# Optimization experiments

Measured on AMD Instinct MI355X. Metric: run time of the kernel, lower is better.

Reference implementation:

```python
import jax, jax.numpy as jnp
import numpy as np

B, S, IN_DIM, P_DIM, H = 2, 2048, 1024, 512, 8
HD = P_DIM // H
N_PENTA = 1024
SCALES = (128, 256, 512)
K_NEIGH = max(16, min(int(S * 0.15), 128))  # adaptive window -> 128
SCALE = 1.0 / float(np.sqrt(HD))
EPS = 1e-5


def _ln(x, g, b):
    mu = jnp.mean(x, axis=-1, keepdims=True)
    var = jnp.mean((x - mu) ** 2, axis=-1, keepdims=True)
    return (x - mu) * jax.lax.rsqrt(var + EPS) * g + b


def setup_inputs() -> dict:
    key = jax.random.key(0)
    ks = list(jax.random.split(key, 6 + 2 * len(SCALES)))
    w = lambda k, shp: jax.random.normal(k, shp, jnp.float32) * 0.02
    inp = {
        'sequence_features': jax.random.normal(ks[0], (B, S, IN_DIM), jnp.float32),
        'shared_pentachora': jax.random.normal(ks[1], (N_PENTA, 5, P_DIM), jnp.float32),
        'shared_positions': jax.random.uniform(ks[2], (N_PENTA,), dtype=jnp.float32),
        'proj_W': w(ks[3], (IN_DIM, P_DIM)), 'proj_b': jnp.zeros((P_DIM,), jnp.float32),
        'ln_g': jnp.ones((P_DIM,), jnp.float32), 'ln_b': jnp.zeros((P_DIM,), jnp.float32),
        'qkv_W': w(ks[4], (P_DIM, 3 * P_DIM)), 'qkv_b': jnp.zeros((3 * P_DIM,), jnp.float32),
        'out_W': w(ks[5], (P_DIM, P_DIM)), 'out_b': jnp.zeros((P_DIM,), jnp.float32),
    }
    i = 6
    for s in SCALES:
        inp[f'w1_{s}'] = w(ks[i], (P_DIM, 2 * s)); inp[f'b1_{s}'] = jnp.zeros((2 * s,), jnp.float32)
        inp[f'g_{s}'] = jnp.ones((2 * s,), jnp.float32); inp[f'bb_{s}'] = jnp.zeros((2 * s,), jnp.float32)
        inp[f'w2_{s}'] = w(ks[i + 1], (2 * s, s)); inp[f'b2_{s}'] = jnp.zeros((s,), jnp.float32)
        i += 2
    return inp


def _attend_one(z_b, pos_b, qkv_W, qkv_b, out_W, out_b):
    # z_b: [S, P_DIM], pos_b: [S]
    qkv = (z_b @ qkv_W + qkv_b).reshape(S, 3, H, HD)
    q = jnp.transpose(qkv[:, 0], (1, 0, 2))  # [H, S, HD]
    k = jnp.transpose(qkv[:, 1], (1, 0, 2))
    v = jnp.transpose(qkv[:, 2], (1, 0, 2))
    dist = jnp.abs(pos_b[:, None] - pos_b[None, :])  # [S, S]
    _, routes = jax.lax.top_k(-dist, K_NEIGH)        # [S, K] nearest in Cantor space
    kg = k[:, routes, :]  # [H, S, K, HD] gathered keys
    vg = v[:, routes, :]
    scores = jnp.einsum('hqd,hqkd->hqk', q, kg) * SCALE
    attn = jax.nn.softmax(scores, axis=-1)
    out = jnp.einsum('hqk,hqkd->hqd', attn, vg)
    out = jnp.transpose(out, (1, 0, 2)).reshape(S, P_DIM)
    return out @ out_W + out_b


def reference(sequence_features, shared_pentachora, shared_positions, proj_W, proj_b, ln_g, ln_b, qkv_W, qkv_b, out_W, out_b, w1_128, b1_128, g_128, bb_128, w2_128, b2_128, w1_256, b1_256, g_256, bb_256, w2_256, b2_256, w1_512, b1_512, g_512, bb_512, w2_512, b2_512):
    # centroids from pentachora vertices, L2-normalized
    cent = shared_pentachora.mean(axis=1)
    cent = cent / jnp.clip(jnp.linalg.norm(cent, axis=-1, keepdims=True), 1e-12)
    # input projection -> LN -> GELU -> L2 normalize
    z = jax.nn.gelu(_ln(sequence_features @ proj_W + proj_b, ln_g, ln_b), approximate=False)
    z = z / jnp.clip(jnp.linalg.norm(z, axis=-1, keepdims=True), 1e-12)
    # match to opinion anchors, inherit Cantor positions
    anchor_ids = jnp.argmax(jnp.einsum('bnd,pd->bnp', z, cent), axis=-1)  # [B, S]
    cantor_positions = shared_positions[anchor_ids]  # [B, S]
    # per-sample geometric sparse attention (vmapped over batch)
    z_att = jax.vmap(_attend_one, in_axes=(0, 0, None, None, None, None))(
        z, cantor_positions, qkv_W, qkv_b, out_W, out_b)  # [B, S, P_DIM]
    pooled = z_att.mean(axis=1)  # [B, P_DIM] (no attention mask)
    scale_params = (
        (w1_128, b1_128, g_128, bb_128, w2_128, b2_128),
        (w1_256, b1_256, g_256, bb_256, w2_256, b2_256),
        (w1_512, b1_512, g_512, bb_512, w2_512, b2_512),
    )
    outs = []
    for (w1, b1, g, bb, w2, b2) in scale_params:
        h = jax.nn.gelu(_ln(pooled @ w1 + b1, g, bb), approximate=False)
        outs.append(h @ w2 + b2)
    return jnp.concatenate(outs, axis=-1)  # [B, 128+256+512] concatenated scale opinions
```

## Files before the change

kernel.cpp:

```cpp
#include <hip/hip_runtime.h>
#include <math.h>

#define DEV __device__ __forceinline__

static constexpr int S_LEN  = 2048;
static constexpr int IN_DIM = 1024;
static constexpr int P_DIM  = 512;
static constexpr int NHEAD  = 8;
static constexpr int HD     = 64;
static constexpr int KN     = 128;

typedef __attribute__((ext_vector_type(8))) short bf16x8;
typedef __attribute__((ext_vector_type(4))) float f32x4;

DEV float gelu_exact(float x) {
    return 0.5f * x * (1.0f + erff(x * 0.70710678118654752440f));
}

DEV short bf_hi(float x) {
    unsigned u = __float_as_uint(x);
    unsigned r = (u + 0x7fffu + ((u >> 16) & 1u)) >> 16;
    return (short)r;
}
DEV float bf_f(short h) { return __uint_as_float(((unsigned)(unsigned short)h) << 16); }

DEV float block_reduce_sum(float v, float* sm4) {
    #pragma unroll
    for (int off = 32; off; off >>= 1) v += __shfl_down(v, off, 64);
    int lane = threadIdx.x & 63, w = threadIdx.x >> 6;
    __syncthreads();
    if (lane == 0) sm4[w] = v;
    __syncthreads();
    return sm4[0] + sm4[1] + sm4[2] + sm4[3];
}

__global__ __launch_bounds__(256) void k_cent(const float* __restrict__ penta,
                                              short* __restrict__ ch,
                                              short* __restrict__ cl) {
    int p = blockIdx.x, t = threadIdx.x;
    __shared__ float sm4[4];
    float c0 = 0.f, c1 = 0.f;
    #pragma unroll
    for (int v = 0; v < 5; v++) {
        const float* row = penta + ((long)p * 5 + v) * P_DIM;
        c0 += row[t];
        c1 += row[t + 256];
    }
    c0 /= 5.0f; c1 /= 5.0f;
    float tot = block_reduce_sum(c0 * c0 + c1 * c1, sm4);
    float n = fmaxf(sqrtf(tot), 1e-12f);
    float v0 = c0 / n, v1 = c1 / n;
    short h0 = bf_hi(v0), h1 = bf_hi(v1);
    ch[p * P_DIM + t]       = h0;
    ch[p * P_DIM + t + 256] = h1;
    cl[p * P_DIM + t]       = bf_hi(v0 - bf_f(h0));
    cl[p * P_DIM + t + 256] = bf_hi(v1 - bf_f(h1));
}

template <int K, int N>
__global__ __launch_bounds__(256) void k_wt(const float* __restrict__ W,
                                            short* __restrict__ WTh,
                                            short* __restrict__ WTl) {
    __shared__ float tile[64][65];
    int bk = blockIdx.x, bn = blockIdx.y;
    int t = threadIdx.x;
    int c = t & 63, r4 = t >> 6;
    #pragma unroll
    for (int i = 0; i < 16; i++) {
        int row = r4 + i * 4;
        tile[row][c] = W[(long)(bk * 64 + row) * N + bn * 64 + c];
    }
    __syncthreads();
    #pragma unroll
    for (int i = 0; i < 16; i++) {
        int n = r4 + i * 4;
        float v = tile[c][n];
        short h = bf_hi(v);
        long o = (long)(bn * 64 + n) * K + bk * 64 + c;
        WTh[o] = h;
        WTl[o] = bf_hi(v - bf_f(h));
    }
}

template <int BM, int K, int N, int EPI, bool SPLITA>
__global__ __launch_bounds__(256) void k_mm(const float* __restrict__ Af,
                                            const short* __restrict__ Ash,
                                            const short* __restrict__ Asl,
                                            const short* __restrict__ BTh,
                                            const short* __restrict__ BTl,
                                            const float* __restrict__ bias,
                                            float* __restrict__ C,
                                            unsigned long long* __restrict__ rowkey) {
    constexpr int TI = (BM + 31) / 32;
    __shared__ short Ah[BM * 40], Al[BM * 40], Bh[128 * 40], Bl[128 * 40];
    int t = threadIdx.x;
    int lane = t & 63, wave = t >> 6;
    int wr = (wave >> 1) * (BM / 2), wc = (wave & 1) * 64;
    int m = lane & 15, quad = lane >> 4;
    int rb = blockIdx.x * BM, cb = blockIdx.y * 128;

    f32x4 acc[TI][4];
    #pragma unroll
    for (int i = 0; i < TI; i++)
        #pragma unroll
        for (int j = 0; j < 4; j++) acc[i][j] = (f32x4){0.f, 0.f, 0.f, 0.f};

    for (int k0 = 0; k0 < K; k0 += 32) {
        __syncthreads();
        if constexpr (SPLITA) {
            constexpr int TOT = BM * 4;
            #pragma unroll
            for (int ps = 0; ps < (TOT + 255) / 256; ps++) {
                int idx = t + ps * 256;
                if (idx < TOT) {
                    int row = idx >> 2, c4 = idx & 3;
                    *(float4*)(Ah + row * 40 + c4 * 8) =
                        *(const float4*)(Ash + (long)(rb + row) * K + k0 + c4 * 8);
                    *(float4*)(Al + row * 40 + c4 * 8) =
                        *(const float4*)(Asl + (long)(rb + row) * K + k0 + c4 * 8);
                }
            }
        } else {
            #pragma unroll
            for (int ps = 0; ps < BM / 32; ps++) {
                int row = (t >> 3) + ps * 32;
                int seg = t & 7;
                float4 v = *(const float4*)(Af + (long)(rb + row) * K + k0 + seg * 4);
                short h0 = bf_hi(v.x), h1 = bf_hi(v.y), h2 = bf_hi(v.z), h3 = bf_hi(v.w);
                short l0 = bf_hi(v.x - bf_f(h0)), l1 = bf_hi(v.y - bf_f(h1));
                short l2 = bf_hi(v.z - bf_f(h2)), l3 = bf_hi(v.w - bf_f(h3));
                *(short4*)(Ah + row * 40 + seg * 4) = make_short4(h0, h1, h2, h3);
                *(short4*)(Al + row * 40 + seg * 4) = make_short4(l0, l1, l2, l3);
            }
        }
        #pragma unroll
        for (int ps = 0; ps < 2; ps++) {
            int row = (t >> 2) + ps * 64;
            int seg = t & 3;
            *(float4*)(Bh + row * 40 + seg * 8) =
                *(const float4*)(BTh + (long)(cb + row) * K + k0 + seg * 8);
            *(float4*)(Bl + row * 40 + seg * 8) =
                *(const float4*)(BTl + (long)(cb + row) * K + k0 + seg * 8);
        }
        __syncthreads();

        bf16x8 ah[TI], al[TI], bh[4], bl[4];
        #pragma unroll
        for (int i = 0; i < TI; i++) {
            ah[i] = *(const bf16x8*)(Ah + (wr + i * 16 + m) * 40 + quad * 8);
            al[i] = *(const bf16x8*)(Al + (wr + i * 16 + m) * 40 + quad * 8);
        }
        #pragma unroll
        for (int j = 0; j < 4; j++) {
            bh[j] = *(const bf16x8*)(Bh + (wc + j * 16 + m) * 40 + quad * 8);
            bl[j] = *(const bf16x8*)(Bl + (wc + j * 16 + m) * 40 + quad * 8);
        }
        #pragma unroll
        for (int i = 0; i < TI; i++)
            #pragma unroll
            for (int j = 0; j < 4; j++) {
                acc[i][j] = __builtin_amdgcn_mfma_f32_16x16x32_bf16(ah[i], bh[j], acc[i][j], 0, 0, 0);
                acc[i][j] = __builtin_amdgcn_mfma_f32_16x16x32_bf16(ah[i], bl[j], acc[i][j], 0, 0, 0);
                acc[i][j] = __builtin_amdgcn_mfma_f32_16x16x32_bf16(al[i], bh[j], acc[i][j], 0, 0, 0);
            }
    }

    if (EPI == 0) {
        #pragma unroll
        for (int i = 0; i < TI; i++) {
            int gr0 = rb + wr + i * 16 + quad * 4;
            #pragma unroll
            for (int j = 0; j < 4; j++) {
                int gc = cb + wc + j * 16 + m;
                float bv = bias[gc];
                #pragma unroll
                for (int r = 0; r < 4; r++)
                    C[(long)(gr0 + r) * N + gc] = acc[i][j][r] + bv;
            }
        }
    } else {
        #pragma unroll
        for (int i = 0; i < TI; i++) {
            #pragma unroll
            for (int r = 0; r < 4; r++) {
                int gr = rb + wr + i * 16 + quad * 4 + r;
                float bv = acc[i][0][r];
                int bp = cb + wc + m;
                #pragma unroll
                for (int j = 1; j < 4; j++) {
                    float v = acc[i][j][r];
                    int p = cb + wc + j * 16 + m;
                    if (v > bv) { bv = v; bp = p; }
                }
                #pragma unroll
                for (int off = 1; off < 16; off <<= 1) {
                    float ov = __shfl_xor(bv, off, 64);
                    int op = __shfl_xor(bp, off, 64);
                    if (ov > bv || (ov == bv && op < bp)) { bv = ov; bp = op; }
                }
                if (m == 0) {
                    unsigned u = __float_as_uint(bv);
                    u = (u & 0x80000000u) ? ~u : (u | 0x80000000u);
                    unsigned long long key =
                        ((unsigned long long)u << 32) | (unsigned)(0xFFFFFFFFu - (unsigned)bp);
                    atomicMax(&rowkey[gr], key);
                }
            }
        }
    }
}

__global__ __launch_bounds__(256) void k_ln_gelu_norm(const float* __restrict__ Zin,
                                                      const float* __restrict__ g,
                                                      const float* __restrict__ b,
                                                      short* __restrict__ z_h,
                                                      short* __restrict__ z_l) {
    long row = blockIdx.x;
    int t = threadIdx.x;
    __shared__ float sm4[4];
    float x0 = Zin[row * P_DIM + t], x1 = Zin[row * P_DIM + t + 256];
    float mu = block_reduce_sum(x0 + x1, sm4) * (1.0f / P_DIM);
    float d0 = x0 - mu, d1 = x1 - mu;
    float var = block_reduce_sum(d0 * d0 + d1 * d1, sm4) * (1.0f / P_DIM);
    float rs = 1.0f / sqrtf(var + 1e-5f);
    float y0 = gelu_exact(d0 * rs * g[t] + b[t]);
    float y1 = gelu_exact(d1 * rs * g[t + 256] + b[t + 256]);
    float nn = block_reduce_sum(y0 * y0 + y1 * y1, sm4);
    float n = fmaxf(sqrtf(nn), 1e-12f);
    float v0 = y0 / n, v1 = y1 / n;
    short h0 = bf_hi(v0), h1 = bf_hi(v1);
    z_h[row * P_DIM + t]       = h0;
    z_h[row * P_DIM + t + 256] = h1;
    z_l[row * P_DIM + t]       = bf_hi(v0 - bf_f(h0));
    z_l[row * P_DIM + t + 256] = bf_hi(v1 - bf_f(h1));
}

__global__ __launch_bounds__(1024) void k_sort(const unsigned long long* __restrict__ rowkey,
                                               const float* __restrict__ spos,
                                               int* __restrict__ order,
                                               float* __restrict__ pos_srt) {
    int b = blockIdx.x, t = threadIdx.x;
    __shared__ unsigned long long key[2048];
    for (int u = 0; u < 2; u++) {
        int i = t + u * 1024;
        unsigned p = 0xFFFFFFFFu - (unsigned)(rowkey[b * 2048 + i] & 0xFFFFFFFFull);
        float pv = spos[p];
        key[i] = (((unsigned long long)__float_as_uint(pv)) << 32) | (unsigned)i;
    }
    __syncthreads();
    for (int k = 2; k <= 2048; k <<= 1) {
        for (int j = k >> 1; j > 0; j >>= 1) {
            for (int u = 0; u < 2; u++) {
                int i = t + u * 1024;
                int l = i ^ j;
                if (l > i) {
                    bool up = ((i & k) == 0);
                    unsigned long long a = key[i], c = key[l];
                    if ((a > c) == up) { key[i] = c; key[l] = a; }
                }
            }
            __syncthreads();
        }
    }
    for (int u = 0; u < 2; u++) {
        int r = t + u * 1024;
        unsigned long long kk = key[r];
        order[b * 2048 + r]   = (int)(kk & 0xffffffffu);
        pos_srt[b * 2048 + r] = __uint_as_float((unsigned)(kk >> 32));
    }
}

__global__ __launch_bounds__(256) void k_routes(const float* __restrict__ pos_srt,
                                                const int* __restrict__ order,
                                                unsigned long long* __restrict__ bmG,
                                                uint2* __restrict__ bounds) {
    int blk = blockIdx.x;
    int b = blk >> 9;
    int t = threadIdx.x;
    int lane = t & 63, wave = t >> 6;
    int r = (blk & 511) * 4 + wave;
    __shared__ float ps[2048];
    __shared__ unsigned short tk[2048];
    for (int u = 0; u < 8; u++) {
        int i = t + u * 256;
        ps[i] = pos_srt[b * 2048 + i];
        tk[i] = (unsigned short)order[b * 2048 + i];
    }
    __syncthreads();

    float pi = ps[r];
    float T = 3e38f;
    #pragma unroll
    for (int a2 = 0; a2 < 2; a2++) {
        int a = lane + a2 * 64;
        int jl = r - a, jr = r + 127 - a;
        if (jl >= 0 && jr <= 2047) {
            float dl = (a > 0)   ? (pi - ps[jl]) : 0.f;
            float dr = (a < 127) ? (ps[jr] - pi) : 0.f;
            T = fminf(T, fmaxf(dl, dr));
        }
    }
    #pragma unroll
    for (int off = 1; off < 64; off <<= 1) T = fminf(T, __shfl_xor(T, off, 64));

    int lo = 0, hi = r;
    while (lo < hi) { int mid = (lo + hi) >> 1; if (pi - ps[mid] <= T) hi = mid; else lo = mid + 1; }
    int mn = lo;
    lo = r; hi = 2047;
    while (lo < hi) { int mid = (lo + hi + 1) >> 1; if (ps[mid] - pi <= T) lo = mid; else hi = mid - 1; }
    int mx = lo;
    int Ls, Rs;
    if (T > 0.f) {
        lo = 0; hi = r;
        while (lo < hi) { int mid = (lo + hi) >> 1; if (pi - ps[mid] < T) hi = mid; else lo = mid + 1; }
        Ls = lo;
        lo = r; hi = 2047;
        while (lo < hi) { int mid = (lo + hi + 1) >> 1; if (ps[mid] - pi < T) lo = mid; else hi = mid - 1; }
        Rs = lo;
    } else { Ls = r + 1; Rs = r - 1; }

    int cnt_strict = (Rs >= Ls) ? (Rs - Ls + 1) : 0;
    int need = 128 - cnt_strict;
    int l0a, l0b, r0a, r0b;
    if (cnt_strict > 0) { l0a = mn; l0b = Ls - 1; r0a = Rs + 1; r0b = mx; }
    else                { l0a = mn; l0b = mx;     r0a = 1;      r0b = 0; }
    int nL = (l0b >= l0a) ? (l0b - l0a + 1) : 0;
    int nR = (r0b >= r0a) ? (r0b - r0a + 1) : 0;
    int tiecount = nL + nR;

    int X = 65535;
    if (need < tiecount) {
        int lo2 = 0, hi2 = 2047;
        while (lo2 < hi2) {
            int mid = (lo2 + hi2) >> 1;
            int cnt = 0;
            for (int e = lane; e < tiecount; e += 64) {
                int j = (e < nL) ? (l0a + e) : (r0a + e - nL);
                cnt += (tk[j] <= mid) ? 1 : 0;
            }
            #pragma unroll
            for (int off = 1; off < 64; off <<= 1) cnt += __shfl_xor(cnt, off, 64);
            if (cnt >= need) hi2 = mid; else lo2 = mid + 1;
        }
        X = lo2;
    }

    int qlo_loc = 1 << 30, qhi_loc = -1;
    if (lane < 32) {
        unsigned long long bits = 0;
        int j0 = lane << 6, j1 = j0 + 63;
        if (cnt_strict > 0) {
            int a0 = max(Ls, j0), a1 = min(Rs, j1);
            if (a0 <= a1) {
                int s = a0 - j0, e = a1 - j0;
                unsigned long long msk = (e - s == 63) ? ~0ull
                                       : (((1ull << (e - s + 1)) - 1) << s);
                bits |= msk;
            }
        }
        int a0 = max(l0a, j0), a1 = min(l0b, j1);
        for (int j = a0; j <= a1; j++) if (tk[j] <= X) bits |= 1ull << (j - j0);
        a0 = max(r0a, j0); a1 = min(r0b, j1);
        for (int j = a0; j <= a1; j++) if (tk[j] <= X) bits |= 1ull << (j - j0);
        if (bits) {
            qlo_loc = j0 + __builtin_ctzll(bits);
            qhi_loc = j0 + 63 - __builtin_clzll(bits);
        }
        bmG[((long)(b * 2048 + r)) * 32 + lane] = bits;
    }
    #pragma unroll
    for (int off = 1; off < 64; off <<= 1) {
        qlo_loc = min(qlo_loc, __shfl_xor(qlo_loc, off, 64));
        qhi_loc = max(qhi_loc, __shfl_xor(qhi_loc, off, 64));
    }
    if (lane == 0)
        bounds[b * 2048 + r] = make_uint2((unsigned)qlo_loc, (unsigned)qhi_loc);
}

__global__ __launch_bounds__(256) void k_kprep(const float* __restrict__ qkv,
                                               const int* __restrict__ order,
                                               short* __restrict__ Ks_h,
                                               short* __restrict__ Ks_l) {
    int b = blockIdx.y;
    int t = threadIdx.x;
    int lr = t >> 5;
    int seg = t & 31;
    int rank = blockIdx.x * 8 + lr;
    int tok = order[b * 2048 + rank];
    const float4* src = (const float4*)qkv + (long)(b * 2048 + tok) * 384 + 128 + seg * 4;
    long dsto = (long)(b * 2048 + rank) * 512 + seg * 16;
    #pragma unroll
    for (int u = 0; u < 4; u++) {
        float4 v = src[u];
        short h0 = bf_hi(v.x), h1 = bf_hi(v.y), h2 = bf_hi(v.z), h3 = bf_hi(v.w);
        *(short4*)(Ks_h + dsto + u * 4) = make_short4(h0, h1, h2, h3);
        *(short4*)(Ks_l + dsto + u * 4) =
            make_short4(bf_hi(v.x - bf_f(h0)), bf_hi(v.y - bf_f(h1)),
                        bf_hi(v.z - bf_f(h2)), bf_hi(v.w - bf_f(h3)));
    }
}

__global__ __launch_bounds__(256) void k_vprep(const float* __restrict__ qkv,
                                               const int* __restrict__ order,
                                               short* __restrict__ Vt_h) {
    __shared__ short tile[64][72];
    int rt = blockIdx.x, dt = blockIdx.y, b = blockIdx.z;
    int t = threadIdx.x;
    int lr = t >> 2;
    int q4 = t & 3;
    int tok = order[b * 2048 + rt * 64 + lr];
    const float4* src = (const float4*)qkv + (long)(b * 2048 + tok) * 384 + 256 + dt * 16;
    #pragma unroll
    for (int u = 0; u < 4; u++) {
        float4 v = src[q4 + u * 4];
        int d0 = (q4 + u * 4) * 4;
        tile[d0 + 0][lr] = bf_hi(v.x);
        tile[d0 + 1][lr] = bf_hi(v.y);
        tile[d0 + 2][lr] = bf_hi(v.z);
        tile[d0 + 3][lr] = bf_hi(v.w);
    }
    __syncthreads();
    int d = t >> 2, c4 = t & 3;
    long o = ((long)(b * 512 + dt * 64 + d)) * 2048 + rt * 64 + c4 * 16;
    #pragma unroll
    for (int j = 0; j < 4; j++)
        *(short4*)(Vt_h + o + j * 4) = make_short4(tile[d][c4 * 16 + j * 4 + 0],
                                                   tile[d][c4 * 16 + j * 4 + 1],
                                                   tile[d][c4 * 16 + j * 4 + 2],
                                                   tile[d][c4 * 16 + j * 4 + 3]);
}

__global__ __launch_bounds__(256) void k_attn(const float* __restrict__ qkv,
                                              const int* __restrict__ order,
                                              const unsigned long long* __restrict__ bmG,
                                              const uint2* __restrict__ bounds,
                                              const short* __restrict__ Ks_h,
                                              const short* __restrict__ Ks_l,
                                              const short* __restrict__ Vt_h,
                                              float* __restrict__ pooledZ) {
    __shared__ __align__(16) char smem[17280];
    short* Pt = (short*)smem;
    unsigned short* cm = (unsigned short*)(smem + 10240);
    float* Opart = (float*)smem;
    float2* ml = (float2*)(smem + 16384);
    int* sh_tok = (int*)(smem + 16896);
    int* sh_lohi = (int*)(smem + 16960);
    float2* sc = (float2*)(smem + 16968);

    int gb = blockIdx.x;
    int b  = gb >> 9;
    int qg = (gb >> 2) & 127;
    int hp = gb & 3;
    int h0 = hp * 2;
    int r0 = qg * 16;
    int t = threadIdx.x;
    int lane = t & 63, wave = t >> 6;
    int rh = wave & 1, hs = wave >> 1;
    int key = lane & 15, quad = lane >> 4;

    const float4* qkvF4 = (const float4*)qkv;

    if (t < 16) sh_tok[t] = order[b * 2048 + r0 + t];
    if (t == 0) { sh_lohi[0] = 1 << 30; sh_lohi[1] = 0; }
    #pragma unroll
    for (int u = 0; u < 8; u++) {
        int e = t + u * 256;
        int c = e >> 4, q = e & 15;
        cm[c * 16 + q] = (unsigned short)(
            (bmG[((long)(b * 2048 + r0 + q)) * 32 + (c >> 2)] >> ((c & 3) * 16)) & 0xFFFF);
    }
    __syncthreads();
    if (t < 16) {
        uint2 bd = bounds[b * 2048 + r0 + t];
        atomicMin(&sh_lohi[0], (int)bd.x);
        atomicMax(&sh_lohi[1], (int)bd.y);
    }

    bf16x8 qh[2], ql[2];
    {
        long tq = (long)(b * 2048 + sh_tok[key]) * 384;
        #pragma unroll
        for (int ks = 0; ks < 2; ks++) {
            float4 v0 = qkvF4[tq + (h0 + hs) * 16 + ks * 8 + quad * 2];
            float4 v1 = qkvF4[tq + (h0 + hs) * 16 + ks * 8 + quad * 2 + 1];
            float vv[8] = {v0.x, v0.y, v0.z, v0.w, v1.x, v1.y, v1.z, v1.w};
            #pragma unroll
            for (int j = 0; j < 8; j++) {
                short hb = bf_hi(vv[j]);
                qh[ks][j] = hb;
                ql[ks][j] = bf_hi(vv[j] - bf_f(hb));
            }
        }
    }
    __syncthreads();
    int lo = sh_lohi[0] & ~63, hi = sh_lohi[1] + 1;

    float mrow[4], lrow[4];
    f32x4 Ont[4];
    #pragma unroll
    for (int r = 0; r < 4; r++) { mrow[r] = -1e30f; lrow[r] = 0.f; }
    #pragma unroll
    for (int nt = 0; nt < 4; nt++) Ont[nt] = (f32x4){0.f, 0.f, 0.f, 0.f};

    short* PtH = Pt + wave * 1280;
    short* PtL = PtH + 640;

    int hd = h0 + hs;
    long kbase = ((long)b * 2048) * 512 + hd * 64 + quad * 8;
    long vbase = ((long)(b * 512 + hd * 64 + key)) * 2048;

    for (int c0 = lo; c0 < hi; c0 += 64) {
        int cb = c0 + rh * 32;
        if (cb >= hi) continue;
        int ch0 = cb >> 4;
        unsigned long long m0 = *(const unsigned long long*)(cm + ch0 * 16 + quad * 4);
        unsigned long long m1 = (ch0 + 1 < 128)
            ? *(const unsigned long long*)(cm + (ch0 + 1) * 16 + quad * 4) : 0ull;
        if (!__any((m0 | m1) != 0ull)) continue;

        long kr0 = kbase + (long)(cb + key) * 512;
        long kr1 = kbase + (long)(cb + 16 + key) * 512;

        f32x4 S0 = (f32x4){0.f,0.f,0.f,0.f}, S1 = (f32x4){0.f,0.f,0.f,0.f};
        #pragma unroll
        for (int ks = 0; ks < 2; ks++) {
            bf16x8 b0h = *(const bf16x8*)(Ks_h + kr0 + ks * 32);
            bf16x8 b0l = *(const bf16x8*)(Ks_l + kr0 + ks * 32);
            bf16x8 b1h = *(const bf16x8*)(Ks_h + kr1 + ks * 32);
            bf16x8 b1l = *(const bf16x8*)(Ks_l + kr1 + ks * 32);
            S0 = __builtin_amdgcn_mfma_f32_16x16x32_bf16(qh[ks], b0h, S0, 0, 0, 0);
            S0 = __builtin_amdgcn_mfma_f32_16x16x32_bf16(qh[ks], b0l, S0, 0, 0, 0);
            S0 = __builtin_amdgcn_mfma_f32_16x16x32_bf16(ql[ks], b0h, S0, 0, 0, 0);
            S1 = __builtin_amdgcn_mfma_f32_16x16x32_bf16(qh[ks], b1h, S1, 0, 0, 0);
            S1 = __builtin_amdgcn_mfma_f32_16x16x32_bf16(qh[ks], b1l, S1, 0, 0, 0);
            S1 = __builtin_amdgcn_mfma_f32_16x16x32_bf16(ql[ks], b1h, S1, 0, 0, 0);
        }
        float s0[4], s1[4], p0[4], p1[4];
        unsigned bit0[4], bit1[4];
        #pragma unroll
        for (int r = 0; r < 4; r++) {
            bit0[r] = (unsigned)((m0 >> (r * 16 + key)) & 1);
            bit1[r] = (unsigned)((m1 >> (r * 16 + key)) & 1);
            s0[r] = bit0[r] ? S0[r] * 0.125f : -1e30f;
            s1[r] = bit1[r] ? S1[r] * 0.125f : -1e30f;
        }
        #pragma unroll
        for (int r = 0; r < 4; r++) {
            float cmax = fmaxf(s0[r], s1[r]);
            cmax = fmaxf(cmax, __shfl_xor(cmax, 1, 64));
            cmax = fmaxf(cmax, __shfl_xor(cmax, 2, 64));
            cmax = fmaxf(cmax, __shfl_xor(cmax, 4, 64));
            cmax = fmaxf(cmax, __shfl_xor(cmax, 8, 64));
            float mn = fmaxf(mrow[r], cmax);
            float alpha = __expf(mrow[r] - mn);
            mrow[r] = mn;
            p0[r] = bit0[r] ? __expf(s0[r] - mn) : 0.f;
            p1[r] = bit1[r] ? __expf(s1[r] - mn) : 0.f;
            float rs = p0[r] + p1[r];
            rs += __shfl_xor(rs, 1, 64);
            rs += __shfl_xor(rs, 2, 64);
            rs += __shfl_xor(rs, 4, 64);
            rs += __shfl_xor(rs, 8, 64);
            lrow[r] = lrow[r] * alpha + rs;
            #pragma unroll
            for (int nt = 0; nt < 4; nt++) Ont[nt][r] *= alpha;
        }
        #pragma unroll
        for (int r = 0; r < 4; r++) {
            short ha = bf_hi(p0[r]);
            PtH[(quad * 4 + r) * 40 + key] = ha;
            PtL[(quad * 4 + r) * 40 + key] = bf_hi(p0[r] - bf_f(ha));
            short hb = bf_hi(p1[r]);
            PtH[(quad * 4 + r) * 40 + 16 + key] = hb;
            PtL[(quad * 4 + r) * 40 + 16 + key] = bf_hi(p1[r] - bf_f(hb));
        }
        bf16x8 pfh = *(const bf16x8*)(PtH + key * 40 + quad * 8);
        bf16x8 pfl = *(const bf16x8*)(PtL + key * 40 + quad * 8);
        #pragma unroll
        for (int nt = 0; nt < 4; nt++) {
            bf16x8 vf = *(const bf16x8*)(Vt_h + vbase + (long)nt * 16 * 2048
                                         + cb + quad * 8);
            Ont[nt] = __builtin_amdgcn_mfma_f32_16x16x32_bf16(pfh, vf, Ont[nt], 0, 0, 0);
            Ont[nt] = __builtin_amdgcn_mfma_f32_16x16x32_bf16(pfl, vf, Ont[nt], 0, 0, 0);
        }
    }

    if (key == 0) {
        #pragma unroll
        for (int r = 0; r < 4; r++)
            ml[(rh * 2 + hs) * 16 + quad * 4 + r] = make_float2(mrow[r], lrow[r]);
    }
    __syncthreads();
    #pragma unroll
    for (int nt = 0; nt < 4; nt++)
        #pragma unroll
        for (int r = 0; r < 4; r++)
            Opart[rh * 2048 + (quad * 4 + r) * 128 + hs * 64 + nt * 16 + key] = Ont[nt][r];

    if (t < 32) {
        int q = t >> 1, hs2 = t & 1;
        float2 a = ml[(0 * 2 + hs2) * 16 + q];
        float2 c = ml[(1 * 2 + hs2) * 16 + q];
        float M = fmaxf(a.x, c.x);
        float w0 = __expf(a.x - M), w1 = __expf(c.x - M);
        float inv = 1.0f / fmaxf(a.y * w0 + c.y * w1, 1e-37f);
        sc[hs2 * 16 + q] = make_float2(w0 * inv, w1 * inv);
    }
    __syncthreads();

    if (t < 128) {
        int d = t, hs2 = d >> 6;
        float s = 0.f;
        #pragma unroll
        for (int q = 0; q < 16; q++) {
            float2 w = sc[hs2 * 16 + q];
            s += Opart[q * 128 + d] * w.x + Opart[2048 + q * 128 + d] * w.y;
        }
        atomicAdd(&pooledZ[b * P_DIM + h0 * HD + d], s);
    }
}

__global__ __launch_bounds__(256) void k_opool(const float* __restrict__ pooledZ,
                                               const float* __restrict__ outW,
                                               const float* __restrict__ outb,
                                               float* __restrict__ pooled) {
    int b = blockIdx.y, t = threadIdx.x;
    int c = blockIdx.x * 256 + t;
    __shared__ float pz[P_DIM];
    pz[t]       = pooledZ[b * P_DIM + t];
    pz[t + 256] = pooledZ[b * P_DIM + t + 256];
    __syncthreads();
    float acc = 0.f;
    #pragma unroll 8
    for (int d = 0; d < P_DIM; d++) acc = fmaf(pz[d], outW[d * P_DIM + c], acc);
    pooled[b * P_DIM + c] = acc + (float)S_LEN * outb[c];
}

__global__ __launch_bounds__(256) void k_exp_fc1(const float* __restrict__ pooled,
                                                 const float* __restrict__ w1_0, const float* __restrict__ b1_0,
                                                 const float* __restrict__ w1_1, const float* __restrict__ b1_1,
                                                 const float* __restrict__ w1_2, const float* __restrict__ b1_2,
                                                 float* __restrict__ h) {
    int t = threadIdx.x, b = blockIdx.y;
    int c = blockIdx.x * 256 + t;
    __shared__ float pl[P_DIM];
    pl[t]       = pooled[b * P_DIM + t]       * (1.0f / S_LEN);
    pl[t + 256] = pooled[b * P_DIM + t + 256] * (1.0f / S_LEN);
    __syncthreads();

    const float* wp; const float* bp; int s2, j;
    if (c < 256)      { wp = w1_0; bp = b1_0; s2 = 256;  j = c; }
    else if (c < 768) { wp = w1_1; bp = b1_1; s2 = 512;  j = c - 256; }
    else              { wp = w1_2; bp = b1_2; s2 = 1024; j = c - 768; }

    const float* p = wp + j;
    float acc = 0.f;
    #pragma unroll 16
    for (int k = 0; k < P_DIM; k++) {
        acc = fmaf(pl[k], *p, acc);
        p += s2;
    }
    h[(long)b * 1792 + c] = acc + bp[j];
}

__global__ __launch_bounds__(256) void k_exp_ln(float* __restrict__ h,
                                                const float* __restrict__ g0, const float* __restrict__ bb0,
                                                const float* __restrict__ g1, const float* __restrict__ bb1,
                                                const float* __restrict__ g2, const float* __restrict__ bb2) {
    int e = blockIdx.x, b = blockIdx.y, t = threadIdx.x;
    __shared__ float sm4[4];
    const int offs[3] = {0, 256, 768};
    const int ns[3]   = {256, 512, 1024};
    const float* gs[3]  = {g0, g1, g2};
    const float* bbs[3] = {bb0, bb1, bb2};
    int n = ns[e];
    float* hp = h + (long)b * 1792 + offs[e];
    const float* g = gs[e]; const float* bb = bbs[e];

    float x[4];
    float loc = 0.f;
    for (int u = 0; u < 4; u++) {
        int j = t + u * 256;
        x[u] = (j < n) ? hp[j] : 0.f;
        loc += x[u];
    }
    float mu = block_reduce_sum(loc, sm4) / (float)n;
    loc = 0.f;
    for (int u = 0; u < 4; u++) {
        int j = t + u * 256;
        if (j < n) { float d = x[u] - mu; loc += d * d; }
    }
    float var = block_reduce_sum(loc, sm4) / (float)n;
    float rs = 1.0f / sqrtf(var + 1e-5f);
    for (int u = 0; u < 4; u++) {
        int j = t + u * 256;
        if (j < n) hp[j] = gelu_exact((x[u] - mu) * rs * g[j] + bb[j]);
    }
}

__global__ __launch_bounds__(256) void k_exp_fc2(const float* __restrict__ h,
                                                 const float* __restrict__ w2_0, const float* __restrict__ b2_0,
                                                 const float* __restrict__ w2_1, const float* __restrict__ b2_1,
                                                 const float* __restrict__ w2_2, const float* __restrict__ b2_2,
                                                 float* __restrict__ out) {
    int t = threadIdx.x, b = blockIdx.y;
    int c = blockIdx.x * 256 + t;
    __shared__ float hs[1792];
    for (int u = 0; u < 7; u++) hs[t + u * 256] = h[(long)b * 1792 + t + u * 256];
    __syncthreads();
    if (c >= 896) return;

    const float* wp; const float* bp; int s2, sN, j, off_h;
    if (c < 128)      { wp = w2_0; bp = b2_0; s2 = 256;  sN = 128; j = c;       off_h = 0; }
    else if (c < 384) { wp = w2_1; bp = b2_1; s2 = 512;  sN = 256; j = c - 128; off_h = 256; }
    else              { wp = w2_2; bp = b2_2; s2 = 1024; sN = 512; j = c - 384; off_h = 768; }

    const float* p = wp + j;
    const float* hh = hs + off_h;
    float acc = 0.f;
    #pragma unroll 16
    for (int k = 0; k < s2; k++) {
        acc = fmaf(hh[k], *p, acc);
        p += sN;
    }
    out[b * 896 + c] = acc + bp[j];
}

extern "C" void kernel_launch(void* const* d_in, const int* in_sizes, int n_in,
                              void* d_out, int out_size, void* d_ws, size_t ws_size,
                              hipStream_t stream) {
    const float* seq   = (const float*)d_in[0];
    const float* penta = (const float*)d_in[1];
    const float* spos  = (const float*)d_in[2];
    const float* projW = (const float*)d_in[3];
    const float* projb = (const float*)d_in[4];
    const float* lng   = (const float*)d_in[5];
    const float* lnb   = (const float*)d_in[6];
    const float* qkvW  = (const float*)d_in[7];
    const float* qkvb  = (const float*)d_in[8];
    const float* outW  = (const float*)d_in[9];
    const float* outb  = (const float*)d_in[10];

    float* ws      = (float*)d_ws;
    float* z_pre   = ws;
    short* z_h     = (short*)(z_pre + 2097152);
    short* z_l     = z_h + 2097152;
    float* qkv     = (float*)(z_l + 2097152);
    float* pooledZ = qkv + 6291456;
    float* pooled  = pooledZ + 4096;
    float* hbuf    = pooled + 1024;
    unsigned long long* rowkey = (unsigned long long*)(hbuf + 4096);
    float* pos_srt = (float*)(rowkey + 4096);
    int*   order   = (int*)(pos_srt + 4096);
    uint2* bounds  = (uint2*)(order + 4096);
    unsigned long long* bmG = (unsigned long long*)(bounds + 4096);
    short* cent_h  = (short*)(bmG + 131072);
    short* cent_l  = cent_h + 524288;
    short* pjWT_h  = cent_l + 524288;
    short* pjWT_l  = pjWT_h + 524288;
    short* qkWT_h  = pjWT_l + 524288;
    short* qkWT_l  = qkWT_h + 786432;

    short* Ks_h = (short*)z_pre;
    short* Ks_l = Ks_h + 2097152;
    short* Vt_h = cent_h;

    k_cent<<<1024, 256, 0, stream>>>(penta, cent_h, cent_l);
    { dim3 g(16, 8);  k_wt<IN_DIM, P_DIM><<<g, 256, 0, stream>>>(projW, pjWT_h, pjWT_l); }
    { dim3 g(8, 24);  k_wt<P_DIM, 3 * P_DIM><<<g, 256, 0, stream>>>(qkvW, qkWT_h, qkWT_l); }

    { dim3 g(128, 4); k_mm<32, IN_DIM, P_DIM, 0, false><<<g, 256, 0, stream>>>(
          seq, nullptr, nullptr, pjWT_h, pjWT_l, projb, z_pre, nullptr); }
    k_ln_gelu_norm<<<4096, 256, 0, stream>>>(z_pre, lng, lnb, z_h, z_l);

    hipMemsetAsync(rowkey, 0, 4096 * sizeof(unsigned long long), stream);
    hipMemsetAsync(pooledZ, 0, 1024 * sizeof(float), stream);
    { dim3 g(128, 8); k_mm<32, P_DIM, 1024, 1, true><<<g, 256, 0, stream>>>(
          nullptr, z_h, z_l, cent_h, cent_l, nullptr, nullptr, rowkey); }
    k_sort<<<2, 1024, 0, stream>>>(rowkey, spos, order, pos_srt);

    { dim3 g(128, 12); k_mm<32, P_DIM, 3 * P_DIM, 0, true><<<g, 256, 0, stream>>>(
          nullptr, z_h, z_l, qkWT_h, qkWT_l, qkvb, qkv, nullptr); }
    k_routes<<<1024, 256, 0, stream>>>(pos_srt, order, bmG, bounds);
    { dim3 g(256, 2); k_kprep<<<g, 256, 0, stream>>>(qkv, order, Ks_h, Ks_l); }
    { dim3 g(32, 8, 2); k_vprep<<<g, 256, 0, stream>>>(qkv, order, Vt_h); }
    k_attn<<<1024, 256, 0, stream>>>(qkv, order, bmG, bounds,
                                     Ks_h, Ks_l, Vt_h, pooledZ);

    { dim3 g(2, 2); k_opool<<<g, 256, 0, stream>>>(pooledZ, outW, outb, pooled); }

    dim3 g1(7, 2);
    k_exp_fc1<<<g1, 256, 0, stream>>>(pooled,
        (const float*)d_in[11], (const float*)d_in[12],
        (const float*)d_in[17], (const float*)d_in[18],
        (const float*)d_in[23], (const float*)d_in[24], hbuf);
    dim3 g2(3, 2);
    k_exp_ln<<<g2, 256, 0, stream>>>(hbuf,
        (const float*)d_in[13], (const float*)d_in[14],
        (const float*)d_in[19], (const float*)d_in[20],
        (const float*)d_in[25], (const float*)d_in[26]);
    dim3 g3(4, 2);
    k_exp_fc2<<<g3, 256, 0, stream>>>(hbuf,
        (const float*)d_in[15], (const float*)d_in[16],
        (const float*)d_in[21], (const float*)d_in[22],
        (const float*)d_in[27], (const float*)d_in[28], (float*)d_out);
}
```

Baseline: 393.0 us.

## Use direct global-to-LDS loads with XOR swizzle and larger GEMM tiles

Rewrites the split-bf16 MFMA GEMM to fetch A and B tiles with global_load_lds straight into an XOR-swizzled shared layout. It doubles the K step to 64 and grows the row tile to 64 or 128, which cuts barriers and register staging per FLOP. The fp32 input projection now takes its bf16 hi/lo operands from a new pre-split kernel that writes into the qkv scratch buffer. This adds an extra pass over the input, and the larger tiles launch fewer blocks and use more LDS.

```diff
diff --git a/kernel.cpp b/kernel.cpp
--- a/kernel.cpp
+++ b/kernel.cpp
@@ -32,6 +32,21 @@
     if (lane == 0) sm4[w] = v;
     __syncthreads();
     return sm4[0] + sm4[1] + sm4[2] + sm4[3];
+}
+
+__global__ __launch_bounds__(256) void k_split(const float* __restrict__ X,
+                                               short* __restrict__ Xh,
+                                               short* __restrict__ Xl) {
+    long base = ((long)blockIdx.x * 256 + threadIdx.x) * 16;
+    #pragma unroll
+    for (int u = 0; u < 4; u++) {
+        float4 v = *(const float4*)(X + base + u * 4);
+        short h0 = bf_hi(v.x), h1 = bf_hi(v.y), h2 = bf_hi(v.z), h3 = bf_hi(v.w);
+        *(short4*)(Xh + base + u * 4) = make_short4(h0, h1, h2, h3);
+        *(short4*)(Xl + base + u * 4) =
+            make_short4(bf_hi(v.x - bf_f(h0)), bf_hi(v.y - bf_f(h1)),
+                        bf_hi(v.z - bf_f(h2)), bf_hi(v.w - bf_f(h3)));
+    }
 }
 
 __global__ __launch_bounds__(256) void k_cent(const float* __restrict__ penta,
@@ -82,22 +97,26 @@
     }
 }
 
-template <int BM, int K, int N, int EPI, bool SPLITA>
-__global__ __launch_bounds__(256) void k_mm(const float* __restrict__ Af,
-                                            const short* __restrict__ Ash,
+template <int BM, int K, int N, int EPI>
+__global__ __launch_bounds__(256) void k_mm(const short* __restrict__ Ash,
                                             const short* __restrict__ Asl,
                                             const short* __restrict__ BTh,
                                             const short* __restrict__ BTl,
                                             const float* __restrict__ bias,
                                             float* __restrict__ C,
                                             unsigned long long* __restrict__ rowkey) {
-    constexpr int TI = (BM + 31) / 32;
-    __shared__ short Ah[BM * 40], Al[BM * 40], Bh[128 * 40], Bl[128 * 40];
+    constexpr int TI  = BM / 32;
+    constexpr int CA  = BM / 8;
+    constexpr int NCH = 2 * CA + 32;
+    __shared__ __align__(128) short AhS[BM * 64], AlS[BM * 64];
+    __shared__ __align__(128) short BhS[128 * 64], BlS[128 * 64];
     int t = threadIdx.x;
     int lane = t & 63, wave = t >> 6;
     int wr = (wave >> 1) * (BM / 2), wc = (wave & 1) * 64;
     int m = lane & 15, quad = lane >> 4;
     int rb = blockIdx.x * BM, cb = blockIdx.y * 128;
+    int r8 = lane >> 3, p8 = lane & 7;
+    int sl = p8 ^ r8;
 
     f32x4 acc[TI][4];
     #pragma unroll
@@ -105,64 +124,57 @@
         #pragma unroll
         for (int j = 0; j < 4; j++) acc[i][j] = (f32x4){0.f, 0.f, 0.f, 0.f};
 
-    for (int k0 = 0; k0 < K; k0 += 32) {
+    for (int k0 = 0; k0 < K; k0 += 64) {
         __syncthreads();
-        if constexpr (SPLITA) {
-            constexpr int TOT = BM * 4;
+        for (int c = wave; c < NCH; c += 4) {
+            const short* src; short* dst;
+            if (c < CA) {
+                src = Ash + (long)(rb + c * 8 + r8) * K + k0 + sl * 8;
+                dst = AhS + c * 512;
+            } else if (c < 2 * CA) {
+                int cc = c - CA;
+                src = Asl + (long)(rb + cc * 8 + r8) * K + k0 + sl * 8;
+                dst = AlS + cc * 512;
+            } else if (c < 2 * CA + 16) {
+                int cc = c - 2 * CA;
+                src = BTh + (long)(cb + cc * 8 + r8) * K + k0 + sl * 8;
+                dst = BhS + cc * 512;
+            } else {
+                int cc = c - 2 * CA - 16;
+                src = BTl + (long)(cb + cc * 8 + r8) * K + k0 + sl * 8;
+                dst = BlS + cc * 512;
+            }
+            __builtin_amdgcn_global_load_lds(
+                (const __attribute__((address_space(1))) unsigned int*)src,
+                (__attribute__((address_space(3))) unsigned int*)dst, 16, 0, 0);
+        }
+        __syncthreads();
+
+        #pragma unroll
+        for (int ks = 0; ks < 2; ks++) {
+            int so = ((ks * 4 + quad) ^ (m & 7)) * 8;
+            bf16x8 ah[TI], al[TI], bh[4], bl[4];
             #pragma unroll
-            for (int ps = 0; ps < (TOT + 255) / 256; ps++) {
-                int idx = t + ps * 256;
-                if (idx < TOT) {
-                    int row = idx >> 2, c4 = idx & 3;
-                    *(float4*)(Ah + row * 40 + c4 * 8) =
-                        *(const float4*)(Ash + (long)(rb + row) * K + k0 + c4 * 8);
-                    *(float4*)(Al + row * 40 + c4 * 8) =
-                        *(const float4*)(Asl + (long)(rb + row) * K + k0 + c4 * 8);
-                }
+            for (int i = 0; i < TI; i++) {
+                int off = (wr + i * 16 + m) * 64 + so;
+                ah[i] = *(const bf16x8*)(AhS + off);
+                al[i] = *(const bf16x8*)(AlS + off);
             }
-        } else {
-            #pragma unroll
-            for (int ps = 0; ps < BM / 32; ps++) {
-                int row = (t >> 3) + ps * 32;
-                int seg = t & 7;
-                float4 v = *(const float4*)(Af + (long)(rb + row) * K + k0 + seg * 4);
-                short h0 = bf_hi(v.x), h1 = bf_hi(v.y), h2 = bf_hi(v.z), h3 = bf_hi(v.w);
-                short l0 = bf_hi(v.x - bf_f(h0)), l1 = bf_hi(v.y - bf_f(h1));
-                short l2 = bf_hi(v.z - bf_f(h2)), l3 = bf_hi(v.w - bf_f(h3));
-                *(short4*)(Ah + row * 40 + seg * 4) = make_short4(h0, h1, h2, h3);
-                *(short4*)(Al + row * 40 + seg * 4) = make_short4(l0, l1, l2, l3);
-            }
-        }
-        #pragma unroll
-        for (int ps = 0; ps < 2; ps++) {
-            int row = (t >> 2) + ps * 64;
-            int seg = t & 3;
-            *(float4*)(Bh + row * 40 + seg * 8) =
-                *(const float4*)(BTh + (long)(cb + row) * K + k0 + seg * 8);
-            *(float4*)(Bl + row * 40 + seg * 8) =
-                *(const float4*)(BTl + (long)(cb + row) * K + k0 + seg * 8);
-        }
-        __syncthreads();
-
-        bf16x8 ah[TI], al[TI], bh[4], bl[4];
-        #pragma unroll
-        for (int i = 0; i < TI; i++) {
-            ah[i] = *(const bf16x8*)(Ah + (wr + i * 16 + m) * 40 + quad * 8);
-            al[i] = *(const bf16x8*)(Al + (wr + i * 16 + m) * 40 + quad * 8);
-        }
-        #pragma unroll
-        for (int j = 0; j < 4; j++) {
-            bh[j] = *(const bf16x8*)(Bh + (wc + j * 16 + m) * 40 + quad * 8);
-            bl[j] = *(const bf16x8*)(Bl + (wc + j * 16 + m) * 40 + quad * 8);
-        }
-        #pragma unroll
-        for (int i = 0; i < TI; i++)
             #pragma unroll
             for (int j = 0; j < 4; j++) {
-                acc[i][j] = __builtin_amdgcn_mfma_f32_16x16x32_bf16(ah[i], bh[j], acc[i][j], 0, 0, 0);
-                acc[i][j] = __builtin_amdgcn_mfma_f32_16x16x32_bf16(ah[i], bl[j], acc[i][j], 0, 0, 0);
-                acc[i][j] = __builtin_amdgcn_mfma_f32_16x16x32_bf16(al[i], bh[j], acc[i][j], 0, 0, 0);
+                int off = (wc + j * 16 + m) * 64 + so;
+                bh[j] = *(const bf16x8*)(BhS + off);
+                bl[j] = *(const bf16x8*)(BlS + off);
             }
+            #pragma unroll
+            for (int i = 0; i < TI; i++)
+                #pragma unroll
+                for (int j = 0; j < 4; j++) {
+                    acc[i][j] = __builtin_amdgcn_mfma_f32_16x16x32_bf16(ah[i], bh[j], acc[i][j], 0, 0, 0);
+                    acc[i][j] = __builtin_amdgcn_mfma_f32_16x16x32_bf16(ah[i], bl[j], acc[i][j], 0, 0, 0);
+                    acc[i][j] = __builtin_amdgcn_mfma_f32_16x16x32_bf16(al[i], bh[j], acc[i][j], 0, 0, 0);
+                }
+        }
     }
 
     if (EPI == 0) {
@@ -761,6 +773,8 @@
     short* qkWT_h  = pjWT_l + 524288;
     short* qkWT_l  = qkWT_h + 786432;
 
+    short* seq_h = (short*)qkv;
+    short* seq_l = seq_h + 4194304;
     short* Ks_h = (short*)z_pre;
     short* Ks_l = Ks_h + 2097152;
     short* Vt_h = cent_h;
@@ -768,19 +782,20 @@
     k_cent<<<1024, 256, 0, stream>>>(penta, cent_h, cent_l);
     { dim3 g(16, 8);  k_wt<IN_DIM, P_DIM><<<g, 256, 0, stream>>>(projW, pjWT_h, pjWT_l); }
     { dim3 g(8, 24);  k_wt<P_DIM, 3 * P_DIM><<<g, 256, 0, stream>>>(qkvW, qkWT_h, qkWT_l); }
-
-    { dim3 g(128, 4); k_mm<32, IN_DIM, P_DIM, 0, false><<<g, 256, 0, stream>>>(
-          seq, nullptr, nullptr, pjWT_h, pjWT_l, projb, z_pre, nullptr); }
+    k_split<<<1024, 256, 0, stream>>>(seq, seq_h, seq_l);
+
+    { dim3 g(64, 4);  k_mm<64, IN_DIM, P_DIM, 0><<<g, 256, 0, stream>>>(
+          seq_h, seq_l, pjWT_h, pjWT_l, projb, z_pre, nullptr); }
     k_ln_gelu_norm<<<4096, 256, 0, stream>>>(z_pre, lng, lnb, z_h, z_l);
 
     hipMemsetAsync(rowkey, 0, 4096 * sizeof(unsigned long long), stream);
     hipMemsetAsync(pooledZ, 0, 1024 * sizeof(float), stream);
-    { dim3 g(128, 8); k_mm<32, P_DIM, 1024, 1, true><<<g, 256, 0, stream>>>(
-          nullptr, z_h, z_l, cent_h, cent_l, nullptr, nullptr, rowkey); }
+    { dim3 g(32, 8);  k_mm<128, P_DIM, 1024, 1><<<g, 256, 0, stream>>>(
+          z_h, z_l, cent_h, cent_l, nullptr, nullptr, rowkey); }
     k_sort<<<2, 1024, 0, stream>>>(rowkey, spos, order, pos_srt);
 
-    { dim3 g(128, 12); k_mm<32, P_DIM, 3 * P_DIM, 0, true><<<g, 256, 0, stream>>>(
-          nullptr, z_h, z_l, qkWT_h, qkWT_l, qkvb, qkv, nullptr); }
+    { dim3 g(32, 12); k_mm<128, P_DIM, 3 * P_DIM, 0><<<g, 256, 0, stream>>>(
+          z_h, z_l, qkWT_h, qkWT_l, qkvb, qkv, nullptr); }
     k_routes<<<1024, 256, 0, stream>>>(pos_srt, order, bmG, bounds);
     { dim3 g(256, 2); k_kprep<<<g, 256, 0, stream>>>(qkv, order, Ks_h, Ks_l); }
     { dim3 g(32, 8, 2); k_vprep<<<g, 256, 0, stream>>>(qkv, order, Vt_h); }
```

New measurement: 393.3 us. About the same (+0.1%).
